# Optimization experiments

Hardware: AMD Instinct MI355X
Metric: run time of the kernel (lower is better)

## Reference

```python
import jax, jax.numpy as jnp
import numpy as np

N_GROUP = 4
TOPK_GROUP = 2
TOP_K = 6
ROUTED_SCALE = 2.0

T, H, E, I = 1024, 1024, 16, 704
SHARED_I = 2 * H  # n_shared_experts * hidden_size


def setup_inputs() -> dict:
    key = jax.random.key(0)
    ks = jax.random.split(key, 10)
    s = 0.02
    return {
        "h": jax.random.normal(ks[0], (T, H), jnp.float32),
        "gate_w": jax.random.normal(ks[1], (E, H), jnp.float32) * s,
        "bias": jax.random.normal(ks[2], (E,), jnp.float32) * 0.1,
        "wg": jax.random.normal(ks[3], (E, H, I), jnp.float32) * s,
        "wu": jax.random.normal(ks[4], (E, H, I), jnp.float32) * s,
        "wd": jax.random.normal(ks[5], (E, I, H), jnp.float32) * s,
        "swg": jax.random.normal(ks[6], (H, SHARED_I), jnp.float32) * s,
        "swu": jax.random.normal(ks[7], (H, SHARED_I), jnp.float32) * s,
        "swd": jax.random.normal(ks[8], (SHARED_I, H), jnp.float32) * s,
    }


def _moe_forward(h, gate_w, bias, wg, wu, wd, swg, swu, swd):
    Tn, Hd = h.shape
    En = gate_w.shape[0]
    per_group = En // N_GROUP

    # shared expert (SwiGLU MLP)
    shared = (jax.nn.silu(h @ swg) * (h @ swu)) @ swd  # [T, H]

    # gate: noaux_tc biased grouped top-k routing (DeepSeek-V3 style)
    logits = h @ gate_w.T                      # [T, E]
    scores = jax.nn.sigmoid(logits)            # [T, E]
    scores_for_choice = scores + bias[None, :]
    grp = scores_for_choice.reshape(Tn, N_GROUP, per_group)
    group_scores = jnp.sum(jax.lax.top_k(grp, 2)[0], axis=-1)   # [T, G] top-2 sum
    _, top_groups = jax.lax.top_k(group_scores, TOPK_GROUP)     # [T, TG]
    gmask = jnp.zeros((Tn, N_GROUP), bool).at[
        jnp.arange(Tn)[:, None], top_groups].set(True)
    emask = jnp.repeat(gmask, per_group, axis=1)                # [T, E]
    masked = jnp.where(emask, scores_for_choice, -jnp.inf)
    _, topk_ids = jax.lax.top_k(masked, TOP_K)                  # [T, K]
    topk_w = jnp.take_along_axis(scores, topk_ids, axis=1)      # weights from unbiased scores
    topk_w = topk_w / jnp.sum(topk_w, axis=-1, keepdims=True)   # norm_topk_prob=True

    # sparse combine weights [T, E]
    cw = jnp.zeros((Tn, En), h.dtype).at[
        jnp.arange(Tn)[:, None], topk_ids].add(topk_w)

    # per-expert SwiGLU MLPs (dense over experts, sparse combine)
    g = jnp.einsum('th,ehi->tei', h, wg)
    u = jnp.einsum('th,ehi->tei', h, wu)
    y = jnp.einsum('tei,eih->teh', jax.nn.silu(g) * u, wd)
    routed = jnp.einsum('te,teh->th', cw, y)

    return routed * ROUTED_SCALE + shared


def reference(h, gate_w, bias, wg, wu, wd, swg, swu, swd):
    return _moe_forward(h, gate_w, bias, wg, wu, wd, swg, swu, swd)
```

## Files before the change

kernel.cpp:

```cpp
#include <hip/hip_runtime.h>
#include <hip/hip_bf16.h>
#include <math.h>

#define TT 1024
#define HH 1024
#define NEXP 16
#define NI 704
#define SI 2048
#define UPMAX 949
#define WDTILES 2816
#define DNSHARED 64
#define DNMAX (DNSHARED + 504)

typedef unsigned short us;
typedef __attribute__((ext_vector_type(8))) __bf16 bf16x8;
typedef __attribute__((ext_vector_type(4))) float f32x4;
typedef __attribute__((ext_vector_type(4))) unsigned short us4;

__device__ __forceinline__ us f2bf(float f) {
  unsigned u = __builtin_bit_cast(unsigned, f);
  u += 0x7fffu + ((u >> 16) & 1u);
  return (us)(u >> 16);
}

__device__ __forceinline__ int ldsOff(int row, int kg) {
  return (row * 4 + (kg ^ ((row >> 1) & 3))) * 16;
}

__device__ __forceinline__ void gl16(const void* g, void* l) {
  __builtin_amdgcn_global_load_lds((const __attribute__((address_space(1))) void*)g,
                                   (__attribute__((address_space(3))) void*)l, 16, 0, 0);
}

__device__ __forceinline__ int chunkMap(int b, int n) {
  int q = n >> 3, r = n & 7;
  int c = b & 7, i = b >> 3;
  int base = (c < r) ? c * (q + 1) : r * (q + 1) + (c - r) * q;
  return base + i;
}

__device__ __forceinline__ void tconv_tile(const float* __restrict__ inz,
                                           us* __restrict__ outz,
                                           int C, int ldo, int r0, int c0,
                                           float (*tile)[65]) {
  int t = threadIdx.x;
  int rr = t >> 4, cc = (t & 15) * 4;
  #pragma unroll
  for (int i = 0; i < 4; ++i) {
    f32x4 v = *reinterpret_cast<const f32x4*>(inz + (size_t)(r0 + rr + i * 16) * C + c0 + cc);
    tile[rr + i*16][cc + 0] = v[0];
    tile[rr + i*16][cc + 1] = v[1];
    tile[rr + i*16][cc + 2] = v[2];
    tile[rr + i*16][cc + 3] = v[3];
  }
  __syncthreads();
  int c = t >> 2, rq = t & 3;
  us o0[8], o1[8];
  #pragma unroll
  for (int j = 0; j < 8; ++j) {
    o0[j] = f2bf(tile[rq * 16 + j][c]);
    o1[j] = f2bf(tile[rq * 16 + 8 + j][c]);
  }
  us* op = outz + (size_t)(c0 + c) * ldo + r0 + rq * 16;
  *reinterpret_cast<us4*>(op)      = *reinterpret_cast<us4*>(&o0[0]);
  *reinterpret_cast<us4*>(op + 4)  = *reinterpret_cast<us4*>(&o0[4]);
  *reinterpret_cast<us4*>(op + 8)  = *reinterpret_cast<us4*>(&o1[0]);
  *reinterpret_cast<us4*>(op + 12) = *reinterpret_cast<us4*>(&o1[4]);
}

__global__ __launch_bounds__(256) void k_prep(
    const float* __restrict__ h, const float* __restrict__ gw,
    const float* __restrict__ bias, float* __restrict__ cw,
    us* __restrict__ hb, unsigned* __restrict__ selpk,
    const float* __restrict__ wg, const float* __restrict__ wu,
    const float* __restrict__ swg, const float* __restrict__ swu,
    us* __restrict__ wgb, us* __restrict__ wub,
    us* __restrict__ swgb, us* __restrict__ swub) {
  __shared__ float tile[64][65];
  __shared__ float lgS[NEXP];
  int b = blockIdx.x;
  int tid = threadIdx.x;
  if (b < 1024) {
    int t = b;
    const float* hr = h + (size_t)t * HH;
    {
      f32x4 v = *reinterpret_cast<const f32x4*>(hr + tid * 4);
      us4 p;
      p[0] = f2bf(v[0]); p[1] = f2bf(v[1]); p[2] = f2bf(v[2]); p[3] = f2bf(v[3]);
      *reinterpret_cast<us4*>(hb + (size_t)t * HH + tid * 4) = p;
    }
    int e = tid >> 4, sub = tid & 15;
    const f32x4* hr4 = reinterpret_cast<const f32x4*>(hr);
    const f32x4* gr4 = reinterpret_cast<const f32x4*>(gw + (size_t)e * HH);
    float acc = 0.f;
    for (int i = sub; i < 256; i += 16) {
      f32x4 a = hr4[i], g = gr4[i];
      acc += a[0]*g[0] + a[1]*g[1] + a[2]*g[2] + a[3]*g[3];
    }
    acc += __shfl_down(acc, 8, 16);
    acc += __shfl_down(acc, 4, 16);
    acc += __shfl_down(acc, 2, 16);
    acc += __shfl_down(acc, 1, 16);
    if (sub == 0) lgS[e] = acc;
    __syncthreads();
    if (tid == 0) {
      float sc[NEXP], s4[NEXP];
      for (int i = 0; i < NEXP; ++i) {
        sc[i] = 1.f / (1.f + expf(-lgS[i]));
        s4[i] = sc[i] + bias[i];
      }
      float gs[4];
      for (int g = 0; g < 4; ++g) {
        float a = s4[4*g], bb = s4[4*g+1], c = s4[4*g+2], d = s4[4*g+3];
        float mx01 = fmaxf(a, bb), mn01 = fminf(a, bb);
        float mx23 = fmaxf(c, d), mn23 = fminf(c, d);
        float top = fmaxf(mx01, mx23);
        float sec = (mx01 >= mx23) ? fmaxf(mn01, mx23) : fmaxf(mn23, mx01);
        gs[g] = top + sec;
      }
      int g1 = 0;
      for (int g = 1; g < 4; ++g) if (gs[g] > gs[g1]) g1 = g;
      int g2 = -1;
      for (int g = 0; g < 4; ++g) { if (g == g1) continue; if (g2 < 0 || gs[g] > gs[g2]) g2 = g; }
      int sel[6];
      bool used[NEXP];
      for (int i = 0; i < NEXP; ++i) used[i] = false;
      float wsum = 0.f;
      for (int it = 0; it < 6; ++it) {
        int best = -1; float bv = 0.f;
        for (int i = 0; i < NEXP; ++i) {
          int grp = i >> 2;
          if ((grp != g1 && grp != g2) || used[i]) continue;
          if (best < 0 || s4[i] > bv) { best = i; bv = s4[i]; }
        }
        used[best] = true;
        sel[it] = best;
        wsum += sc[best];
      }
      float inv = 2.0f / wsum;
      unsigned pk = 0;
      for (int it = 0; it < 6; ++it) {
        pk |= (unsigned)sel[it] << (it * 4);
        cw[(size_t)t * NEXP + sel[it]] = sc[sel[it]] * inv;
      }
      selpk[t] = pk;
    }
    return;
  }
  b -= 1024;
  if (b < 2816) {
    int z = b / 176, r = b % 176;
    tconv_tile(wg + (size_t)z * HH * NI, wgb + (size_t)z * NI * HH,
               NI, HH, (r / 11) * 64, (r % 11) * 64, tile);
    return;
  }
  b -= 2816;
  if (b < 2816) {
    int z = b / 176, r = b % 176;
    tconv_tile(wu + (size_t)z * HH * NI, wub + (size_t)z * NI * HH,
               NI, HH, (r / 11) * 64, (r % 11) * 64, tile);
    return;
  }
  b -= 2816;
  if (b < 512) {
    tconv_tile(swg, swgb, SI, HH, (b >> 5) * 64, (b & 31) * 64, tile);
    return;
  }
  b -= 512;
  {
    tconv_tile(swu, swub, SI, HH, (b >> 5) * 64, (b & 31) * 64, tile);
  }
}

__global__ void k_scan(const unsigned* __restrict__ selpk,
                       int* __restrict__ cnt, int* __restrict__ list,
                       int* __restrict__ wlUp, int* __restrict__ wlDn,
                       int* __restrict__ totals) {
  int t = threadIdx.x;
  int w = t >> 6, l = t & 63;
  unsigned pk = selpk[t];
  unsigned short flags = 0;
  #pragma unroll
  for (int j = 0; j < 6; ++j) flags |= (unsigned short)(1u << ((pk >> (j * 4)) & 15));
  __shared__ int wc[16][16];
  __shared__ int pre[16][16];
  __shared__ int tiles_s[16], upo[16], dno[16], totR[2];
  #pragma unroll
  for (int e = 0; e < 16; ++e) {
    unsigned long long bal = __ballot((flags >> e) & 1);
    if (l == 0) wc[w][e] = __popcll(bal);
  }
  __syncthreads();
  if (t < 16) {
    int s = 0;
    for (int ww = 0; ww < 16; ++ww) { pre[ww][t] = s; s += wc[ww][t]; }
    cnt[t] = s;
    tiles_s[t] = (s + 127) >> 7;
  }
  __syncthreads();
  if (t < 16) {
    int uo = 0, dn = 0;
    for (int e2 = 0; e2 < t; ++e2) { uo += 11 * tiles_s[e2]; dn += 8 * tiles_s[e2]; }
    upo[t] = uo; dno[t] = dn;
    if (t == 15) { totR[0] = uo + 11 * tiles_s[15]; totR[1] = dn + 8 * tiles_s[15]; }
  }
  __syncthreads();
  {
    int te = tiles_s[w];
    for (int i = l; i < 11 * te; i += 64) {
      int nt = i / te, mt = i - nt * te;
      wlUp[upo[w] + i] = ((w * 11 + nt) << 3) | mt;
    }
    for (int i = l; i < 8 * te; i += 64) {
      int nt = i / te, mt = i - nt * te;
      wlDn[dno[w] + i] = ((w * 8 + nt) << 3) | mt;
    }
  }
  if (w == 0) {
    for (int j = l; j < 256; j += 64)
      wlUp[totR[0] + j] = ((176 + (j >> 3)) << 3) | (j & 7);
  }
  if (t == 0) { totals[0] = totR[0] + 256; totals[1] = totR[1]; }
  unsigned long long lmask = (l == 0) ? 0ull : ((~0ull) >> (64 - l));
  #pragma unroll
  for (int e = 0; e < 16; ++e) {
    bool f = (flags >> e) & 1;
    unsigned long long bal = __ballot(f);
    if (f) {
      int rank = __popcll(bal & lmask);
      int j = 0;
      #pragma unroll
      for (int jj = 0; jj < 6; ++jj) j += (((pk >> (jj * 4)) & 15) == (unsigned)e) ? jj : 0;
      list[(e << 10) + pre[w][e] + rank] = (t << 3) | j;
    }
  }
}

__global__ void k_tconvS(const float* __restrict__ swd, us* __restrict__ swdT) {
  __shared__ float tile[64][65];
  int b = blockIdx.x;
  tconv_tile(swd, swdT, HH, SI, (b >> 4) * 64, (b & 15) * 64, tile);
}

__global__ __launch_bounds__(256) void k_upT(
    const us* __restrict__ hb,
    const us* __restrict__ wgb, const us* __restrict__ wub,
    const us* __restrict__ swgb, const us* __restrict__ swub,
    const float* __restrict__ cw, const int* __restrict__ list,
    const int* __restrict__ cnt, const int* __restrict__ wlUp,
    const int* __restrict__ totals,
    us* __restrict__ cact_r, us* __restrict__ cact_s,
    const float* __restrict__ wd, us* __restrict__ wdbT) {
  __shared__ __align__(16) char ldsb[32768];
  int tid = threadIdx.x;
  if ((int)blockIdx.x >= UPMAX) {
    int b = blockIdx.x - UPMAX;
    int z = b / 176, r = b % 176;
    tconv_tile(wd + (size_t)z * NI * HH, wdbT + (size_t)z * HH * NI,
               HH, NI, (r / 16) * 64, (r % 16) * 64,
               reinterpret_cast<float(*)[65]>(ldsb));
    return;
  }
  int tot = totals[0];
  if ((int)blockIdx.x >= tot) return;
  int item = wlUp[chunkMap(blockIdx.x, tot)];
  int group = item >> 3, mt = item & 7;
  int t0 = mt * 128;
  bool routed = group < 176;
  int e = 0, n0, cntE = TT;
  const us *bgBase, *buBase;
  if (routed) {
    e = group / 11;
    n0 = (group - e * 11) * 64;
    cntE = cnt[e];
    bgBase = wgb + (size_t)e * NI * HH;
    buBase = wub + (size_t)e * NI * HH;
  } else {
    n0 = (group - 176) * 64;
    bgBase = swgb;
    buBase = swub;
  }
  int w = tid >> 6, l = tid & 63;
  int wm = w >> 1, wn = w & 1;
  int lr = l & 15, lg2 = l >> 4;

  int rowA = tid >> 2;
  int kg = (tid & 3) ^ ((rowA >> 1) & 3);
  int tok0 = t0 + rowA, tok1 = t0 + 64 + rowA;
  if (routed) {
    tok0 = (tok0 < cntE) ? (list[(e << 10) + tok0] >> 3) : 0;
    tok1 = (tok1 < cntE) ? (list[(e << 10) + tok1] >> 3) : 0;
  }
  const us* aS0 = hb + (size_t)tok0 * HH + kg * 8;
  const us* aS1 = hb + (size_t)tok1 * HH + kg * 8;
  const us* gS  = bgBase + (size_t)(n0 + rowA) * HH + kg * 8;
  const us* uS  = buBase + (size_t)(n0 + rowA) * HH + kg * 8;

  f32x4 accG[4][2] = {};
  f32x4 accU[4][2] = {};

  int wslot = w * 1024;
  auto stage = [&](char* buf) {
    char* b = buf + wslot;
    gl16(aS0, b);
    gl16(aS1, b + 4096);
    gl16(gS,  b + 8192);
    gl16(uS,  b + 12288);
    aS0 += 32; aS1 += 32; gS += 32; uS += 32;
  };

  char* bufR = ldsb;
  char* bufW = ldsb + 16384;
  stage(bufR);
  __syncthreads();
  #pragma unroll 2
  for (int ki = 0; ki < 32; ++ki) {
    if (ki < 31) stage(bufW);
    bf16x8 af[4], bg[2], bu[2];
    #pragma unroll
    for (int rf = 0; rf < 4; ++rf)
      af[rf] = *reinterpret_cast<const bf16x8*>(bufR + ldsOff(wm * 64 + rf * 16 + lr, lg2));
    #pragma unroll
    for (int cf = 0; cf < 2; ++cf) {
      int n = wn * 32 + cf * 16 + lr;
      bg[cf] = *reinterpret_cast<const bf16x8*>(bufR + 8192  + ldsOff(n, lg2));
      bu[cf] = *reinterpret_cast<const bf16x8*>(bufR + 12288 + ldsOff(n, lg2));
    }
    __builtin_amdgcn_s_setprio(1);
    #pragma unroll
    for (int rf = 0; rf < 4; ++rf)
      #pragma unroll
      for (int cf = 0; cf < 2; ++cf) {
        accG[rf][cf] = __builtin_amdgcn_mfma_f32_16x16x32_bf16(af[rf], bg[cf], accG[rf][cf], 0, 0, 0);
        accU[rf][cf] = __builtin_amdgcn_mfma_f32_16x16x32_bf16(af[rf], bu[cf], accU[rf][cf], 0, 0, 0);
      }
    __builtin_amdgcn_s_setprio(0);
    __syncthreads();
    char* tp = bufR; bufR = bufW; bufW = tp;
  }
  #pragma unroll
  for (int rf = 0; rf < 4; ++rf)
    #pragma unroll
    for (int cf = 0; cf < 2; ++cf)
      #pragma unroll
      for (int r = 0; r < 4; ++r) {
        int row = wm * 64 + rf * 16 + lg2 * 4 + r;
        int col = wn * 32 + cf * 16 + lr;
        float g = accG[rf][cf][r], u = accU[rf][cf][r];
        float act = g / (1.f + __expf(-g)) * u;
        if (routed) {
          int slot = t0 + row;
          if (slot < cntE) {
            int packed = list[(e << 10) + slot];
            float scl = cw[(size_t)(packed >> 3) * NEXP + e];
            cact_r[((size_t)(e << 10) + slot) * NI + n0 + col] = f2bf(act * scl);
          }
        } else {
          cact_s[(size_t)(t0 + row) * SI + n0 + col] = f2bf(act);
        }
      }
}

__global__ __launch_bounds__(256) void k_down(
    const us* __restrict__ cact_r, const us* __restrict__ cact_s,
    const us* __restrict__ wdbT, const us* __restrict__ swdT,
    const int* __restrict__ list, const int* __restrict__ cnt,
    const int* __restrict__ wlDn, const int* __restrict__ totals,
    float* __restrict__ part, float* __restrict__ out) {
  __shared__ __align__(16) char ldsb[32768];
  int tid = threadIdx.x;
  int b = blockIdx.x;
  bool routed;
  int e = 0, nt, mt, kiter, Ksrc, cntE = TT;
  const us *Ab, *Bb;
  if (b < DNSHARED) {
    routed = false;
    nt = b & 7;
    mt = b >> 3;
    kiter = 64;
    Ksrc = SI;
    Ab = cact_s;
    Bb = swdT;
  } else {
    routed = true;
    int rb = b - DNSHARED;
    int tot = totals[1];
    if (rb >= tot) return;
    int item = wlDn[chunkMap(rb, tot)];
    int group = item >> 3;
    mt = item & 7;
    e = group >> 3; nt = group & 7;
    cntE = cnt[e];
    kiter = NI / 32;
    Ksrc = NI;
    Ab = cact_r + (size_t)e * 1024 * NI;
    Bb = wdbT + (size_t)e * 1024 * NI;
  }
  int t0 = mt * 128;
  int n0 = nt * 128;
  int w = tid >> 6, l = tid & 63;
  int wm = w >> 1, wn = w & 1;
  int lr = l & 15, lg2 = l >> 4;

  int rowA = tid >> 2;
  int kg = (tid & 3) ^ ((rowA >> 1) & 3);
  const us* aS0 = Ab + (size_t)(t0 + rowA) * Ksrc + kg * 8;
  const us* aS1 = Ab + (size_t)(t0 + 64 + rowA) * Ksrc + kg * 8;
  const us* bS0 = Bb + (size_t)(n0 + rowA) * Ksrc + kg * 8;
  const us* bS1 = Bb + (size_t)(n0 + 64 + rowA) * Ksrc + kg * 8;

  f32x4 acc[4][4] = {};

  int wslot = w * 1024;
  auto stage = [&](char* buf) {
    char* bp = buf + wslot;
    gl16(aS0, bp);
    gl16(aS1, bp + 4096);
    gl16(bS0, bp + 8192);
    gl16(bS1, bp + 12288);
    aS0 += 32; aS1 += 32; bS0 += 32; bS1 += 32;
  };

  char* bufR = ldsb;
  char* bufW = ldsb + 16384;
  stage(bufR);
  __syncthreads();
  for (int ki = 0; ki < kiter; ++ki) {
    if (ki + 1 < kiter) stage(bufW);
    bf16x8 af[4], bb[4];
    #pragma unroll
    for (int rf = 0; rf < 4; ++rf)
      af[rf] = *reinterpret_cast<const bf16x8*>(bufR + ldsOff(wm * 64 + rf * 16 + lr, lg2));
    #pragma unroll
    for (int cf = 0; cf < 4; ++cf)
      bb[cf] = *reinterpret_cast<const bf16x8*>(bufR + 8192 + ldsOff(wn * 64 + cf * 16 + lr, lg2));
    __builtin_amdgcn_s_setprio(1);
    #pragma unroll
    for (int rf = 0; rf < 4; ++rf)
      #pragma unroll
      for (int cf = 0; cf < 4; ++cf)
        acc[rf][cf] = __builtin_amdgcn_mfma_f32_16x16x32_bf16(af[rf], bb[cf], acc[rf][cf], 0, 0, 0);
    __builtin_amdgcn_s_setprio(0);
    __syncthreads();
    char* tp = bufR; bufR = bufW; bufW = tp;
  }
  #pragma unroll
  for (int rf = 0; rf < 4; ++rf)
    #pragma unroll
    for (int cf = 0; cf < 4; ++cf)
      #pragma unroll
      for (int r = 0; r < 4; ++r) {
        int row = wm * 64 + rf * 16 + lg2 * 4 + r;
        int col = wn * 64 + cf * 16 + lr;
        if (routed) {
          int slot = t0 + row;
          if (slot < cntE) {
            int packed = list[(e << 10) + slot];
            int t = packed >> 3, j = packed & 7;
            part[((size_t)t * 6 + j) * 1024 + n0 + col] = acc[rf][cf][r];
          }
        } else {
          out[(size_t)(t0 + row) * HH + n0 + col] = acc[rf][cf][r];
        }
      }
}

__global__ void k_reduce(const float* __restrict__ part, float* __restrict__ out) {
  int i = (blockIdx.x * blockDim.x + threadIdx.x) * 4;
  int t = i >> 10, hh = i & 1023;
  f32x4 s = *reinterpret_cast<const f32x4*>(out + i);
  #pragma unroll
  for (int j = 0; j < 6; ++j)
    s += *reinterpret_cast<const f32x4*>(part + ((size_t)t * 6 + j) * 1024 + hh);
  *reinterpret_cast<f32x4*>(out + i) = s;
}

#define HB_OFF    0ULL
#define CW_OFF    2097152ULL
#define CNT_OFF   2162688ULL
#define SELPK_OFF 2166784ULL
#define LIST_OFF  2170880ULL
#define WLUP_OFF  2236416ULL
#define WLDN_OFF  2244608ULL
#define TOT_OFF   2252800ULL
#define CACTR_OFF 2260992ULL
#define CACTS_OFF 25329664ULL
#define WGB_OFF   29523968ULL
#define WUB_OFF   52592640ULL
#define SWGB_OFF  75661312ULL
#define SWUB_OFF  79855616ULL
#define WDBT_OFF  84049920ULL
#define SWDT_OFF  SWGB_OFF
#define PART_OFF  WGB_OFF

extern "C" void kernel_launch(void* const* d_in, const int* in_sizes, int n_in,
                              void* d_out, int out_size, void* d_ws, size_t ws_size,
                              hipStream_t stream) {
  const float* h    = (const float*)d_in[0];
  const float* gw   = (const float*)d_in[1];
  const float* bias = (const float*)d_in[2];
  const float* wg   = (const float*)d_in[3];
  const float* wu   = (const float*)d_in[4];
  const float* wd   = (const float*)d_in[5];
  const float* swg  = (const float*)d_in[6];
  const float* swu  = (const float*)d_in[7];
  const float* swd  = (const float*)d_in[8];
  float* out = (float*)d_out;

  char* ws = (char*)d_ws;
  us*       hb     = (us*)(ws + HB_OFF);
  float*    cw     = (float*)(ws + CW_OFF);
  int*      cnt    = (int*)(ws + CNT_OFF);
  unsigned* selpk  = (unsigned*)(ws + SELPK_OFF);
  int*      list   = (int*)(ws + LIST_OFF);
  int*      wlUp   = (int*)(ws + WLUP_OFF);
  int*      wlDn   = (int*)(ws + WLDN_OFF);
  int*      totals = (int*)(ws + TOT_OFF);
  us*       cact_r = (us*)(ws + CACTR_OFF);
  us*       cact_s = (us*)(ws + CACTS_OFF);
  us*       wgb    = (us*)(ws + WGB_OFF);
  us*       wub    = (us*)(ws + WUB_OFF);
  us*       swgb   = (us*)(ws + SWGB_OFF);
  us*       swub   = (us*)(ws + SWUB_OFF);
  us*       wdbT   = (us*)(ws + WDBT_OFF);
  us*       swdT   = (us*)(ws + SWDT_OFF);
  float*    part   = (float*)(ws + PART_OFF);

  k_prep<<<7680, 256, 0, stream>>>(h, gw, bias, cw, hb, selpk,
                                   wg, wu, swg, swu, wgb, wub, swgb, swub);
  k_scan<<<1, 1024, 0, stream>>>(selpk, cnt, list, wlUp, wlDn, totals);

  k_upT<<<UPMAX + WDTILES, 256, 0, stream>>>(hb, wgb, wub, swgb, swub, cw, list,
                                             cnt, wlUp, totals, cact_r, cact_s,
                                             wd, wdbT);

  k_tconvS<<<512, 256, 0, stream>>>(swd, swdT);

  k_down<<<DNMAX, 256, 0, stream>>>(cact_r, cact_s, wdbT, swdT, list, cnt,
                                    wlDn, totals, part, out);
  k_reduce<<<1024, 256, 0, stream>>>(part, out);
}
```

Before: 156.9 us.

## Triple-buffer GEMM k-loops with vmcnt waits; split gating and fuse scan into weight conversion

The up and down GEMM kernels move from double to triple buffering in LDS (48 KiB), issuing loads two stages ahead and waiting with explicit vmcnt counts and raw barriers instead of __syncthreads. This is meant to hide global-load latency behind MFMA work. Gating now runs in its own kernel, and the expert-count scan becomes the last block of a new 1024-thread weight-conversion kernel, which uses a simpler one-element-per-thread transpose. The larger LDS footprint may lower occupancy, and the hand-written vmcnt counts depend on the exact number of loads issued per stage.

```diff
diff --git a/kernel.cpp b/kernel.cpp
--- a/kernel.cpp
+++ b/kernel.cpp
@@ -68,123 +68,137 @@
   *reinterpret_cast<us4*>(op + 12) = *reinterpret_cast<us4*>(&o1[4]);
 }
 
-__global__ __launch_bounds__(256) void k_prep(
+__device__ __forceinline__ void tconv1k(const float* __restrict__ inz,
+                                        us* __restrict__ outz,
+                                        int C, int ldo, int r0, int c0,
+                                        float (*tile)[65]) {
+  int t = threadIdx.x;
+  int rr = t >> 4, cc = (t & 15) * 4;
+  f32x4 v = *reinterpret_cast<const f32x4*>(inz + (size_t)(r0 + rr) * C + c0 + cc);
+  tile[rr][cc + 0] = v[0]; tile[rr][cc + 1] = v[1];
+  tile[rr][cc + 2] = v[2]; tile[rr][cc + 3] = v[3];
+  __syncthreads();
+  int c = t >> 4, rq = t & 15;
+  us4 o;
+  #pragma unroll
+  for (int j = 0; j < 4; ++j) o[j] = f2bf(tile[rq * 4 + j][c]);
+  *reinterpret_cast<us4*>(outz + (size_t)(c0 + c) * ldo + r0 + rq * 4) = o;
+}
+
+__global__ __launch_bounds__(256) void k_gate(
     const float* __restrict__ h, const float* __restrict__ gw,
     const float* __restrict__ bias, float* __restrict__ cw,
-    us* __restrict__ hb, unsigned* __restrict__ selpk,
+    us* __restrict__ hb, unsigned* __restrict__ selpk) {
+  __shared__ float lgS[NEXP];
+  int t = blockIdx.x;
+  int tid = threadIdx.x;
+  const float* hr = h + (size_t)t * HH;
+  {
+    f32x4 v = *reinterpret_cast<const f32x4*>(hr + tid * 4);
+    us4 p;
+    p[0] = f2bf(v[0]); p[1] = f2bf(v[1]); p[2] = f2bf(v[2]); p[3] = f2bf(v[3]);
+    *reinterpret_cast<us4*>(hb + (size_t)t * HH + tid * 4) = p;
+  }
+  int e = tid >> 4, sub = tid & 15;
+  const f32x4* hr4 = reinterpret_cast<const f32x4*>(hr);
+  const f32x4* gr4 = reinterpret_cast<const f32x4*>(gw + (size_t)e * HH);
+  float acc = 0.f;
+  for (int i = sub; i < 256; i += 16) {
+    f32x4 a = hr4[i], g = gr4[i];
+    acc += a[0]*g[0] + a[1]*g[1] + a[2]*g[2] + a[3]*g[3];
+  }
+  acc += __shfl_down(acc, 8, 16);
+  acc += __shfl_down(acc, 4, 16);
+  acc += __shfl_down(acc, 2, 16);
+  acc += __shfl_down(acc, 1, 16);
+  if (sub == 0) lgS[e] = acc;
+  __syncthreads();
+  if (tid == 0) {
+    float sc[NEXP], s4[NEXP];
+    for (int i = 0; i < NEXP; ++i) {
+      sc[i] = 1.f / (1.f + expf(-lgS[i]));
+      s4[i] = sc[i] + bias[i];
+    }
+    float gs[4];
+    for (int g = 0; g < 4; ++g) {
+      float a = s4[4*g], bb = s4[4*g+1], c = s4[4*g+2], d = s4[4*g+3];
+      float mx01 = fmaxf(a, bb), mn01 = fminf(a, bb);
+      float mx23 = fmaxf(c, d), mn23 = fminf(c, d);
+      float top = fmaxf(mx01, mx23);
+      float sec = (mx01 >= mx23) ? fmaxf(mn01, mx23) : fmaxf(mn23, mx01);
+      gs[g] = top + sec;
+    }
+    int g1 = 0;
+    for (int g = 1; g < 4; ++g) if (gs[g] > gs[g1]) g1 = g;
+    int g2 = -1;
+    for (int g = 0; g < 4; ++g) { if (g == g1) continue; if (g2 < 0 || gs[g] > gs[g2]) g2 = g; }
+    int sel[6];
+    bool used[NEXP];
+    for (int i = 0; i < NEXP; ++i) used[i] = false;
+    float wsum = 0.f;
+    for (int it = 0; it < 6; ++it) {
+      int best = -1; float bv = 0.f;
+      for (int i = 0; i < NEXP; ++i) {
+        int grp = i >> 2;
+        if ((grp != g1 && grp != g2) || used[i]) continue;
+        if (best < 0 || s4[i] > bv) { best = i; bv = s4[i]; }
+      }
+      used[best] = true;
+      sel[it] = best;
+      wsum += sc[best];
+    }
+    float inv = 2.0f / wsum;
+    unsigned pk = 0;
+    for (int it = 0; it < 6; ++it) {
+      pk |= (unsigned)sel[it] << (it * 4);
+      cw[(size_t)t * NEXP + sel[it]] = sc[sel[it]] * inv;
+    }
+    selpk[t] = pk;
+  }
+}
+
+__global__ __launch_bounds__(1024) void k_prepW(
     const float* __restrict__ wg, const float* __restrict__ wu,
     const float* __restrict__ swg, const float* __restrict__ swu,
     us* __restrict__ wgb, us* __restrict__ wub,
-    us* __restrict__ swgb, us* __restrict__ swub) {
+    us* __restrict__ swgb, us* __restrict__ swub,
+    const unsigned* __restrict__ selpk,
+    int* __restrict__ cnt, int* __restrict__ list,
+    int* __restrict__ wlUp, int* __restrict__ wlDn, int* __restrict__ totals) {
   __shared__ float tile[64][65];
-  __shared__ float lgS[NEXP];
+  __shared__ int wc[16][16];
+  __shared__ int pre[16][16];
+  __shared__ int tiles_s[16], upo[16], dno[16], totR[2];
   int b = blockIdx.x;
-  int tid = threadIdx.x;
-  if (b < 1024) {
-    int t = b;
-    const float* hr = h + (size_t)t * HH;
-    {
-      f32x4 v = *reinterpret_cast<const f32x4*>(hr + tid * 4);
-      us4 p;
-      p[0] = f2bf(v[0]); p[1] = f2bf(v[1]); p[2] = f2bf(v[2]); p[3] = f2bf(v[3]);
-      *reinterpret_cast<us4*>(hb + (size_t)t * HH + tid * 4) = p;
-    }
-    int e = tid >> 4, sub = tid & 15;
-    const f32x4* hr4 = reinterpret_cast<const f32x4*>(hr);
-    const f32x4* gr4 = reinterpret_cast<const f32x4*>(gw + (size_t)e * HH);
-    float acc = 0.f;
-    for (int i = sub; i < 256; i += 16) {
-      f32x4 a = hr4[i], g = gr4[i];
-      acc += a[0]*g[0] + a[1]*g[1] + a[2]*g[2] + a[3]*g[3];
-    }
-    acc += __shfl_down(acc, 8, 16);
-    acc += __shfl_down(acc, 4, 16);
-    acc += __shfl_down(acc, 2, 16);
-    acc += __shfl_down(acc, 1, 16);
-    if (sub == 0) lgS[e] = acc;
-    __syncthreads();
-    if (tid == 0) {
-      float sc[NEXP], s4[NEXP];
-      for (int i = 0; i < NEXP; ++i) {
-        sc[i] = 1.f / (1.f + expf(-lgS[i]));
-        s4[i] = sc[i] + bias[i];
-      }
-      float gs[4];
-      for (int g = 0; g < 4; ++g) {
-        float a = s4[4*g], bb = s4[4*g+1], c = s4[4*g+2], d = s4[4*g+3];
-        float mx01 = fmaxf(a, bb), mn01 = fminf(a, bb);
-        float mx23 = fmaxf(c, d), mn23 = fminf(c, d);
-        float top = fmaxf(mx01, mx23);
-        float sec = (mx01 >= mx23) ? fmaxf(mn01, mx23) : fmaxf(mn23, mx01);
-        gs[g] = top + sec;
-      }
-      int g1 = 0;
-      for (int g = 1; g < 4; ++g) if (gs[g] > gs[g1]) g1 = g;
-      int g2 = -1;
-      for (int g = 0; g < 4; ++g) { if (g == g1) continue; if (g2 < 0 || gs[g] > gs[g2]) g2 = g; }
-      int sel[6];
-      bool used[NEXP];
-      for (int i = 0; i < NEXP; ++i) used[i] = false;
-      float wsum = 0.f;
-      for (int it = 0; it < 6; ++it) {
-        int best = -1; float bv = 0.f;
-        for (int i = 0; i < NEXP; ++i) {
-          int grp = i >> 2;
-          if ((grp != g1 && grp != g2) || used[i]) continue;
-          if (best < 0 || s4[i] > bv) { best = i; bv = s4[i]; }
-        }
-        used[best] = true;
-        sel[it] = best;
-        wsum += sc[best];
-      }
-      float inv = 2.0f / wsum;
-      unsigned pk = 0;
-      for (int it = 0; it < 6; ++it) {
-        pk |= (unsigned)sel[it] << (it * 4);
-        cw[(size_t)t * NEXP + sel[it]] = sc[sel[it]] * inv;
-      }
-      selpk[t] = pk;
-    }
-    return;
-  }
-  b -= 1024;
   if (b < 2816) {
     int z = b / 176, r = b % 176;
-    tconv_tile(wg + (size_t)z * HH * NI, wgb + (size_t)z * NI * HH,
-               NI, HH, (r / 11) * 64, (r % 11) * 64, tile);
+    tconv1k(wg + (size_t)z * HH * NI, wgb + (size_t)z * NI * HH,
+            NI, HH, (r / 11) * 64, (r % 11) * 64, tile);
     return;
   }
   b -= 2816;
   if (b < 2816) {
     int z = b / 176, r = b % 176;
-    tconv_tile(wu + (size_t)z * HH * NI, wub + (size_t)z * NI * HH,
-               NI, HH, (r / 11) * 64, (r % 11) * 64, tile);
+    tconv1k(wu + (size_t)z * HH * NI, wub + (size_t)z * NI * HH,
+            NI, HH, (r / 11) * 64, (r % 11) * 64, tile);
     return;
   }
   b -= 2816;
   if (b < 512) {
-    tconv_tile(swg, swgb, SI, HH, (b >> 5) * 64, (b & 31) * 64, tile);
+    tconv1k(swg, swgb, SI, HH, (b >> 5) * 64, (b & 31) * 64, tile);
     return;
   }
   b -= 512;
-  {
-    tconv_tile(swu, swub, SI, HH, (b >> 5) * 64, (b & 31) * 64, tile);
-  }
-}
-
-__global__ void k_scan(const unsigned* __restrict__ selpk,
-                       int* __restrict__ cnt, int* __restrict__ list,
-                       int* __restrict__ wlUp, int* __restrict__ wlDn,
-                       int* __restrict__ totals) {
+  if (b < 512) {
+    tconv1k(swu, swub, SI, HH, (b >> 5) * 64, (b & 31) * 64, tile);
+    return;
+  }
   int t = threadIdx.x;
   int w = t >> 6, l = t & 63;
   unsigned pk = selpk[t];
   unsigned short flags = 0;
   #pragma unroll
   for (int j = 0; j < 6; ++j) flags |= (unsigned short)(1u << ((pk >> (j * 4)) & 15));
-  __shared__ int wc[16][16];
-  __shared__ int pre[16][16];
-  __shared__ int tiles_s[16], upo[16], dno[16], totR[2];
   #pragma unroll
   for (int e = 0; e < 16; ++e) {
     unsigned long long bal = __ballot((flags >> e) & 1);
@@ -251,7 +265,7 @@
     const int* __restrict__ totals,
     us* __restrict__ cact_r, us* __restrict__ cact_s,
     const float* __restrict__ wd, us* __restrict__ wdbT) {
-  __shared__ __align__(16) char ldsb[32768];
+  __shared__ __align__(16) char ldsb[49152];
   int tid = threadIdx.x;
   if ((int)blockIdx.x >= UPMAX) {
     int b = blockIdx.x - UPMAX;
@@ -309,22 +323,31 @@
     aS0 += 32; aS1 += 32; gS += 32; uS += 32;
   };
 
-  char* bufR = ldsb;
-  char* bufW = ldsb + 16384;
-  stage(bufR);
-  __syncthreads();
-  #pragma unroll 2
+  char* bA = ldsb;
+  char* bB = ldsb + 16384;
+  char* bC = ldsb + 32768;
+  stage(bA);
+  stage(bB);
   for (int ki = 0; ki < 32; ++ki) {
-    if (ki < 31) stage(bufW);
+    if (ki < 30) {
+      stage(bC);
+      asm volatile("s_waitcnt vmcnt(8)" ::: "memory");
+    } else if (ki == 30) {
+      asm volatile("s_waitcnt vmcnt(4)" ::: "memory");
+    } else {
+      asm volatile("s_waitcnt vmcnt(0)" ::: "memory");
+    }
+    __builtin_amdgcn_s_barrier();
+    asm volatile("" ::: "memory");
     bf16x8 af[4], bg[2], bu[2];
     #pragma unroll
     for (int rf = 0; rf < 4; ++rf)
-      af[rf] = *reinterpret_cast<const bf16x8*>(bufR + ldsOff(wm * 64 + rf * 16 + lr, lg2));
+      af[rf] = *reinterpret_cast<const bf16x8*>(bA + ldsOff(wm * 64 + rf * 16 + lr, lg2));
     #pragma unroll
     for (int cf = 0; cf < 2; ++cf) {
       int n = wn * 32 + cf * 16 + lr;
-      bg[cf] = *reinterpret_cast<const bf16x8*>(bufR + 8192  + ldsOff(n, lg2));
-      bu[cf] = *reinterpret_cast<const bf16x8*>(bufR + 12288 + ldsOff(n, lg2));
+      bg[cf] = *reinterpret_cast<const bf16x8*>(bA + 8192  + ldsOff(n, lg2));
+      bu[cf] = *reinterpret_cast<const bf16x8*>(bA + 12288 + ldsOff(n, lg2));
     }
     __builtin_amdgcn_s_setprio(1);
     #pragma unroll
@@ -335,8 +358,9 @@
         accU[rf][cf] = __builtin_amdgcn_mfma_f32_16x16x32_bf16(af[rf], bu[cf], accU[rf][cf], 0, 0, 0);
       }
     __builtin_amdgcn_s_setprio(0);
-    __syncthreads();
-    char* tp = bufR; bufR = bufW; bufW = tp;
+    __builtin_amdgcn_s_barrier();
+    asm volatile("" ::: "memory");
+    char* tp = bA; bA = bB; bB = bC; bC = tp;
   }
   #pragma unroll
   for (int rf = 0; rf < 4; ++rf)
@@ -367,7 +391,7 @@
     const int* __restrict__ list, const int* __restrict__ cnt,
     const int* __restrict__ wlDn, const int* __restrict__ totals,
     float* __restrict__ part, float* __restrict__ out) {
-  __shared__ __align__(16) char ldsb[32768];
+  __shared__ __align__(16) char ldsb[49152];
   int tid = threadIdx.x;
   int b = blockIdx.x;
   bool routed;
@@ -421,19 +445,29 @@
     aS0 += 32; aS1 += 32; bS0 += 32; bS1 += 32;
   };
 
-  char* bufR = ldsb;
-  char* bufW = ldsb + 16384;
-  stage(bufR);
-  __syncthreads();
+  char* bA = ldsb;
+  char* bB = ldsb + 16384;
+  char* bC = ldsb + 32768;
+  stage(bA);
+  stage(bB);
   for (int ki = 0; ki < kiter; ++ki) {
-    if (ki + 1 < kiter) stage(bufW);
+    if (ki + 2 < kiter) {
+      stage(bC);
+      asm volatile("s_waitcnt vmcnt(8)" ::: "memory");
+    } else if (ki + 2 == kiter) {
+      asm volatile("s_waitcnt vmcnt(4)" ::: "memory");
+    } else {
+      asm volatile("s_waitcnt vmcnt(0)" ::: "memory");
+    }
+    __builtin_amdgcn_s_barrier();
+    asm volatile("" ::: "memory");
     bf16x8 af[4], bb[4];
     #pragma unroll
     for (int rf = 0; rf < 4; ++rf)
-      af[rf] = *reinterpret_cast<const bf16x8*>(bufR + ldsOff(wm * 64 + rf * 16 + lr, lg2));
+      af[rf] = *reinterpret_cast<const bf16x8*>(bA + ldsOff(wm * 64 + rf * 16 + lr, lg2));
     #pragma unroll
     for (int cf = 0; cf < 4; ++cf)
-      bb[cf] = *reinterpret_cast<const bf16x8*>(bufR + 8192 + ldsOff(wn * 64 + cf * 16 + lr, lg2));
+      bb[cf] = *reinterpret_cast<const bf16x8*>(bA + 8192 + ldsOff(wn * 64 + cf * 16 + lr, lg2));
     __builtin_amdgcn_s_setprio(1);
     #pragma unroll
     for (int rf = 0; rf < 4; ++rf)
@@ -441,8 +475,9 @@
       for (int cf = 0; cf < 4; ++cf)
         acc[rf][cf] = __builtin_amdgcn_mfma_f32_16x16x32_bf16(af[rf], bb[cf], acc[rf][cf], 0, 0, 0);
     __builtin_amdgcn_s_setprio(0);
-    __syncthreads();
-    char* tp = bufR; bufR = bufW; bufW = tp;
+    __builtin_amdgcn_s_barrier();
+    asm volatile("" ::: "memory");
+    char* tp = bA; bA = bB; bB = bC; bC = tp;
   }
   #pragma unroll
   for (int rf = 0; rf < 4; ++rf)
@@ -526,9 +561,9 @@
   us*       swdT   = (us*)(ws + SWDT_OFF);
   float*    part   = (float*)(ws + PART_OFF);
 
-  k_prep<<<7680, 256, 0, stream>>>(h, gw, bias, cw, hb, selpk,
-                                   wg, wu, swg, swu, wgb, wub, swgb, swub);
-  k_scan<<<1, 1024, 0, stream>>>(selpk, cnt, list, wlUp, wlDn, totals);
+  k_gate<<<1024, 256, 0, stream>>>(h, gw, bias, cw, hb, selpk);
+  k_prepW<<<6657, 1024, 0, stream>>>(wg, wu, swg, swu, wgb, wub, swgb, swub,
+                                     selpk, cnt, list, wlUp, wlDn, totals);
 
   k_upT<<<UPMAX + WDTILES, 256, 0, stream>>>(hb, wgb, wub, swgb, swub, cw, list,
                                              cnt, wlUp, totals, cact_r, cact_s,
```

Result: slower. 161.0 us (+2.6%).

## Load MFMA operands directly from global memory instead of LDS staging

Applied to the files above, without the earlier changes.

Both GEMM kernels (up-projection and down-projection) drop the double-buffered LDS staging via global_load_lds and the per-iteration barriers. Each wave now reads its bf16x8 MFMA fragments straight from global memory through per-row pointers, and launch bounds are raised to 3 blocks per CU. The aim is to remove LDS traffic and synchronisation overhead and to raise occupancy. The cost is that data shared between waves is no longer reused through LDS, so global and L2 traffic roughly doubles, and the loads are narrow strided 16-byte accesses with no software prefetch overlap.

```diff
diff --git a/kernel.cpp b/kernel.cpp
--- a/kernel.cpp
+++ b/kernel.cpp
@@ -21,15 +21,6 @@
   unsigned u = __builtin_bit_cast(unsigned, f);
   u += 0x7fffu + ((u >> 16) & 1u);
   return (us)(u >> 16);
-}
-
-__device__ __forceinline__ int ldsOff(int row, int kg) {
-  return (row * 4 + (kg ^ ((row >> 1) & 3))) * 16;
-}
-
-__device__ __forceinline__ void gl16(const void* g, void* l) {
-  __builtin_amdgcn_global_load_lds((const __attribute__((address_space(1))) void*)g,
-                                   (__attribute__((address_space(3))) void*)l, 16, 0, 0);
 }
 
 __device__ __forceinline__ int chunkMap(int b, int n) {
@@ -242,7 +233,7 @@
   tconv_tile(swd, swdT, HH, SI, (b >> 4) * 64, (b & 15) * 64, tile);
 }
 
-__global__ __launch_bounds__(256) void k_upT(
+__global__ __launch_bounds__(256, 3) void k_upT(
     const us* __restrict__ hb,
     const us* __restrict__ wgb, const us* __restrict__ wub,
     const us* __restrict__ swgb, const us* __restrict__ swub,
@@ -251,14 +242,13 @@
     const int* __restrict__ totals,
     us* __restrict__ cact_r, us* __restrict__ cact_s,
     const float* __restrict__ wd, us* __restrict__ wdbT) {
-  __shared__ __align__(16) char ldsb[32768];
+  __shared__ float tile[64][65];
   int tid = threadIdx.x;
   if ((int)blockIdx.x >= UPMAX) {
     int b = blockIdx.x - UPMAX;
     int z = b / 176, r = b % 176;
     tconv_tile(wd + (size_t)z * NI * HH, wdbT + (size_t)z * HH * NI,
-               HH, NI, (r / 16) * 64, (r % 16) * 64,
-               reinterpret_cast<float(*)[65]>(ldsb));
+               HH, NI, (r / 16) * 64, (r % 16) * 64, tile);
     return;
   }
   int tot = totals[0];
@@ -284,47 +274,35 @@
   int wm = w >> 1, wn = w & 1;
   int lr = l & 15, lg2 = l >> 4;
 
-  int rowA = tid >> 2;
-  int kg = (tid & 3) ^ ((rowA >> 1) & 3);
-  int tok0 = t0 + rowA, tok1 = t0 + 64 + rowA;
-  if (routed) {
-    tok0 = (tok0 < cntE) ? (list[(e << 10) + tok0] >> 3) : 0;
-    tok1 = (tok1 < cntE) ? (list[(e << 10) + tok1] >> 3) : 0;
-  }
-  const us* aS0 = hb + (size_t)tok0 * HH + kg * 8;
-  const us* aS1 = hb + (size_t)tok1 * HH + kg * 8;
-  const us* gS  = bgBase + (size_t)(n0 + rowA) * HH + kg * 8;
-  const us* uS  = buBase + (size_t)(n0 + rowA) * HH + kg * 8;
+  const us* aP[4];
+  #pragma unroll
+  for (int rf = 0; rf < 4; ++rf) {
+    int row = t0 + wm * 64 + rf * 16 + lr;
+    int tok = routed ? ((row < cntE) ? (list[(e << 10) + row] >> 3) : 0) : row;
+    aP[rf] = hb + (size_t)tok * HH + lg2 * 8;
+  }
+  const us* bgP[2];
+  const us* buP[2];
+  #pragma unroll
+  for (int cf = 0; cf < 2; ++cf) {
+    int n = n0 + wn * 32 + cf * 16 + lr;
+    bgP[cf] = bgBase + (size_t)n * HH + lg2 * 8;
+    buP[cf] = buBase + (size_t)n * HH + lg2 * 8;
+  }
 
   f32x4 accG[4][2] = {};
   f32x4 accU[4][2] = {};
 
-  int wslot = w * 1024;
-  auto stage = [&](char* buf) {
-    char* b = buf + wslot;
-    gl16(aS0, b);
-    gl16(aS1, b + 4096);
-    gl16(gS,  b + 8192);
-    gl16(uS,  b + 12288);
-    aS0 += 32; aS1 += 32; gS += 32; uS += 32;
-  };
-
-  char* bufR = ldsb;
-  char* bufW = ldsb + 16384;
-  stage(bufR);
-  __syncthreads();
-  #pragma unroll 2
+  #pragma unroll 4
   for (int ki = 0; ki < 32; ++ki) {
-    if (ki < 31) stage(bufW);
     bf16x8 af[4], bg[2], bu[2];
     #pragma unroll
     for (int rf = 0; rf < 4; ++rf)
-      af[rf] = *reinterpret_cast<const bf16x8*>(bufR + ldsOff(wm * 64 + rf * 16 + lr, lg2));
+      af[rf] = *reinterpret_cast<const bf16x8*>(aP[rf] + ki * 32);
     #pragma unroll
     for (int cf = 0; cf < 2; ++cf) {
-      int n = wn * 32 + cf * 16 + lr;
-      bg[cf] = *reinterpret_cast<const bf16x8*>(bufR + 8192  + ldsOff(n, lg2));
-      bu[cf] = *reinterpret_cast<const bf16x8*>(bufR + 12288 + ldsOff(n, lg2));
+      bg[cf] = *reinterpret_cast<const bf16x8*>(bgP[cf] + ki * 32);
+      bu[cf] = *reinterpret_cast<const bf16x8*>(buP[cf] + ki * 32);
     }
     __builtin_amdgcn_s_setprio(1);
     #pragma unroll
@@ -335,8 +313,6 @@
         accU[rf][cf] = __builtin_amdgcn_mfma_f32_16x16x32_bf16(af[rf], bu[cf], accU[rf][cf], 0, 0, 0);
       }
     __builtin_amdgcn_s_setprio(0);
-    __syncthreads();
-    char* tp = bufR; bufR = bufW; bufW = tp;
   }
   #pragma unroll
   for (int rf = 0; rf < 4; ++rf)
@@ -361,13 +337,12 @@
       }
 }
 
-__global__ __launch_bounds__(256) void k_down(
+__global__ __launch_bounds__(256, 3) void k_down(
     const us* __restrict__ cact_r, const us* __restrict__ cact_s,
     const us* __restrict__ wdbT, const us* __restrict__ swdT,
     const int* __restrict__ list, const int* __restrict__ cnt,
     const int* __restrict__ wlDn, const int* __restrict__ totals,
     float* __restrict__ part, float* __restrict__ out) {
-  __shared__ __align__(16) char ldsb[32768];
   int tid = threadIdx.x;
   int b = blockIdx.x;
   bool routed;
@@ -402,38 +377,30 @@
   int wm = w >> 1, wn = w & 1;
   int lr = l & 15, lg2 = l >> 4;
 
-  int rowA = tid >> 2;
-  int kg = (tid & 3) ^ ((rowA >> 1) & 3);
-  const us* aS0 = Ab + (size_t)(t0 + rowA) * Ksrc + kg * 8;
-  const us* aS1 = Ab + (size_t)(t0 + 64 + rowA) * Ksrc + kg * 8;
-  const us* bS0 = Bb + (size_t)(n0 + rowA) * Ksrc + kg * 8;
-  const us* bS1 = Bb + (size_t)(n0 + 64 + rowA) * Ksrc + kg * 8;
+  const us* aP[4];
+  const us* bP[4];
+  #pragma unroll
+  for (int rf = 0; rf < 4; ++rf)
+    aP[rf] = Ab + (size_t)(t0 + wm * 64 + rf * 16 + lr) * Ksrc + lg2 * 8;
+  #pragma unroll
+  for (int cf = 0; cf < 4; ++cf)
+    bP[cf] = Bb + (size_t)(n0 + wn * 64 + cf * 16 + lr) * Ksrc + lg2 * 8;
 
   f32x4 acc[4][4] = {};
 
-  int wslot = w * 1024;
-  auto stage = [&](char* buf) {
-    char* bp = buf + wslot;
-    gl16(aS0, bp);
-    gl16(aS1, bp + 4096);
-    gl16(bS0, bp + 8192);
-    gl16(bS1, bp + 12288);
-    aS0 += 32; aS1 += 32; bS0 += 32; bS1 += 32;
-  };
-
-  char* bufR = ldsb;
-  char* bufW = ldsb + 16384;
-  stage(bufR);
-  __syncthreads();
+  #pragma unroll 2
   for (int ki = 0; ki < kiter; ++ki) {
-    if (ki + 1 < kiter) stage(bufW);
     bf16x8 af[4], bb[4];
     #pragma unroll
     for (int rf = 0; rf < 4; ++rf)
-      af[rf] = *reinterpret_cast<const bf16x8*>(bufR + ldsOff(wm * 64 + rf * 16 + lr, lg2));
+      af[rf] = *reinterpret_cast<const bf16x8*>(aP[rf]);
     #pragma unroll
     for (int cf = 0; cf < 4; ++cf)
-      bb[cf] = *reinterpret_cast<const bf16x8*>(bufR + 8192 + ldsOff(wn * 64 + cf * 16 + lr, lg2));
+      bb[cf] = *reinterpret_cast<const bf16x8*>(bP[cf]);
+    #pragma unroll
+    for (int rf = 0; rf < 4; ++rf) aP[rf] += 32;
+    #pragma unroll
+    for (int cf = 0; cf < 4; ++cf) bP[cf] += 32;
     __builtin_amdgcn_s_setprio(1);
     #pragma unroll
     for (int rf = 0; rf < 4; ++rf)
@@ -441,8 +408,6 @@
       for (int cf = 0; cf < 4; ++cf)
         acc[rf][cf] = __builtin_amdgcn_mfma_f32_16x16x32_bf16(af[rf], bb[cf], acc[rf][cf], 0, 0, 0);
     __builtin_amdgcn_s_setprio(0);
-    __syncthreads();
-    char* tp = bufR; bufR = bufW; bufW = tp;
   }
   #pragma unroll
   for (int rf = 0; rf < 4; ++rf)
```

Measured after the change: 281.5 us. 79.4% more time.
